# Kernel optimization log

Hardware: AMD Instinct MI355X
Metric: run time of the kernel (lower is better)

## Reference

```python
import jax, jax.numpy as jnp
import numpy as np


def setup_inputs() -> dict:
    key = jax.random.key(0)
    k1, k2 = jax.random.split(key)
    input_tensor = jax.random.normal(k1, (32, 128, 64, 64), dtype=jnp.float32)
    weights = jax.random.normal(k2, (256, 128, 3, 3), dtype=jnp.float32) * 0.05
    return {"input_tensor": input_tensor, "weights": weights}


def reference(input_tensor, weights):
    # Valid-padding, stride-1, no-bias direct conv2d (NCHW x OIHW -> NCHW),
    # identical math to the quintuple-loop slice*weight sum in the original.
    return jax.lax.conv_general_dilated(
        input_tensor,
        weights,
        window_strides=(1, 1),
        padding="VALID",
        dimension_numbers=("NCHW", "OIHW", "NCHW"),
    )
```

## Files before the change

kernel.cpp:

```cpp
#include <hip/hip_runtime.h>
#include <hip/hip_bf16.h>

#define N_IMG 32
#define CIN   128
#define INH   64
#define INW   64
#define COUT  256
#define OH    62
#define OW    62

typedef short          bf16x8 __attribute__((ext_vector_type(8)));
typedef unsigned short u16x8  __attribute__((ext_vector_type(8)));
typedef float          f32x4  __attribute__((ext_vector_type(4)));
typedef float          f32x2  __attribute__((ext_vector_type(2)));

__device__ __forceinline__ unsigned short f2bf(float x) {
    unsigned int u = __float_as_uint(x);
    u += 0x7fffu + ((u >> 16) & 1u);
    return (unsigned short)(u >> 16);
}

__device__ __forceinline__ void gload_lds16(const void* g, void* l) {
    __builtin_amdgcn_global_load_lds(
        (const __attribute__((address_space(1))) unsigned int*)g,
        (__attribute__((address_space(3))) unsigned int*)l, 16, 0, 0);
}

__global__ void wt_transform_kernel(const float* __restrict__ Wsrc,
                                    unsigned short* __restrict__ WT) {
    int idx = blockIdx.x * 256 + threadIdx.x;
    int i   = idx & 7;
    int co  = (idx >> 3) & 255;
    int cgk = idx >> 11;
    int cg  = cgk & 15;
    int khw = cgk >> 4;
    int kh  = khw / 3, kw = khw - 3 * kh;
    int ci  = cg * 8 + i;
    WT[idx] = f2bf(Wsrc[co * (CIN * 9) + ci * 9 + kh * 3 + kw]);
}

__global__ __launch_bounds__(256)
void in_transform_kernel(const float* __restrict__ In,
                         unsigned short* __restrict__ TIn) {
    __shared__ float T[32][66];
    const int bid = blockIdx.x;
    const int ih  = bid & 63;
    const int cb  = (bid >> 6) & 3;
    const int img = bid >> 8;

    {
        const int r  = threadIdx.x >> 3;
        const int c0 = (threadIdx.x & 7) * 8;
        const float* p = In + (((size_t)(img * CIN + cb * 32 + r)) * INH + ih) * INW + c0;
        f32x4 a = *(const f32x4*)p;
        f32x4 b = *(const f32x4*)(p + 4);
        *(f32x2*)&T[r][c0 + 0] = f32x2{a[0], a[1]};
        *(f32x2*)&T[r][c0 + 2] = f32x2{a[2], a[3]};
        *(f32x2*)&T[r][c0 + 4] = f32x2{b[0], b[1]};
        *(f32x2*)&T[r][c0 + 6] = f32x2{b[2], b[3]};
    }
    __syncthreads();

    const int c  = threadIdx.x;
    const int iw = c >> 2;
    const int cg = (c & 3) ^ ((iw >> 1) & 3);
    u16x8 v;
#pragma unroll
    for (int i = 0; i < 8; ++i) v[i] = f2bf(T[cg * 8 + i][iw]);
    *(u16x8*)&TIn[((size_t)bid * 256 + c) * 8] = v;
}

__global__ __launch_bounds__(256, 4)
void conv_mfma_bf16_kernel(const unsigned short* __restrict__ TIn,
                           const unsigned short* __restrict__ WT,
                           float* __restrict__ Out) {
    __shared__ unsigned short Lin[2][2112];

    const int g   = blockIdx.x;
    const int f   = (g & 7) * 248 + (g >> 3);
    const int img = f / OH;
    const int oh  = f - img * OH;

    const int tid  = threadIdx.x;
    const int wave = tid >> 6;
    const int lane = tid & 63;
    const int q    = lane >> 4;
    const int ml   = lane & 15;
    const int co_base = wave * 64;

    const unsigned short* tin_base = TIn + (size_t)img * (4 * 64 * 2048);
    const bf16x8* WTv = (const bf16x8*)WT;
    const int wlane = q * 256 + co_base + ml;

    int xoff[3][4];
#pragma unroll
    for (int kw = 0; kw < 3; ++kw)
#pragma unroll
        for (int ni = 0; ni < 4; ++ni) {
            const int r = ni * 16 + ml + kw;
            xoff[kw][ni] = r * 32 + ((q ^ ((r >> 1) & 3)) << 3);
        }

    f32x4 acc[4][4];
    const f32x4 zero = {0.f, 0.f, 0.f, 0.f};
#pragma unroll
    for (int a = 0; a < 4; ++a)
#pragma unroll
        for (int b = 0; b < 4; ++b) acc[a][b] = zero;

    gload_lds16(tin_base + oh * 2048 + tid * 8, &Lin[0][wave * 512]);
    if (tid < 64) ((unsigned int*)&Lin[tid >> 5][64 * 32])[tid & 31] = 0u;
    __syncthreads();

#pragma unroll
    for (int s = 0; s < 12; ++s) {
        const int cur = s & 1;
        if (s < 11) {
            const int s1 = s + 1;
            const unsigned short* src =
                tin_base + ((s1 & 3) * 64 + oh + (s1 >> 2)) * 2048;
            gload_lds16(src + tid * 8, &Lin[cur ^ 1][wave * 512]);
        }
        const int kh = s >> 2, cb = s & 3;
#pragma unroll
        for (int kw = 0; kw < 3; ++kw) {
            const int khw = kh * 3 + kw;
            const bf16x8* wbase = WTv + (khw * 16 + cb * 4) * 256;
            bf16x8 wf[4], xf[4];
#pragma unroll
            for (int mi = 0; mi < 4; ++mi)
                wf[mi] = wbase[wlane + mi * 16];
#pragma unroll
            for (int ni = 0; ni < 4; ++ni)
                xf[ni] = *(const bf16x8*)&Lin[cur][xoff[kw][ni]];
#pragma unroll
            for (int mi = 0; mi < 4; ++mi)
#pragma unroll
                for (int ni = 0; ni < 4; ++ni)
                    acc[mi][ni] = __builtin_amdgcn_mfma_f32_16x16x32_bf16(
                        wf[mi], xf[ni], acc[mi][ni], 0, 0, 0);
        }
        __syncthreads();
    }

#pragma unroll
    for (int mi = 0; mi < 4; ++mi) {
#pragma unroll
        for (int r = 0; r < 4; ++r) {
            const int co = co_base + mi * 16 + q * 4 + r;
            float* op = Out + ((img * COUT + co) * OH + oh) * OW;
#pragma unroll
            for (int ni = 0; ni < 4; ++ni) {
                const int ow = ni * 16 + ml;
                if (ow < OW) op[ow] = acc[mi][ni][r];
            }
        }
    }
}

__global__ __launch_bounds__(256, 2)
void conv_mfma_fp32_kernel(const float* __restrict__ In,
                           const unsigned short* __restrict__ WT,
                           float* __restrict__ Out) {
    __shared__ unsigned short Lin[66 * 32];

    const int oh   = blockIdx.x;
    const int img  = blockIdx.y;
    const int tid  = threadIdx.x;
    const int wave = tid >> 6;
    const int lane = tid & 63;
    const int q    = lane >> 4;
    const int ml   = lane & 15;
    const int co_base = wave * 64;

    f32x4 acc[4][4];
    const f32x4 zero = {0.f, 0.f, 0.f, 0.f};
#pragma unroll
    for (int a = 0; a < 4; ++a)
#pragma unroll
        for (int b = 0; b < 4; ++b) acc[a][b] = zero;

    if (tid < 32) ((unsigned int*)&Lin[64 * 32])[tid] = 0u;

    const int s_iw = tid & 63;
    const int s_cg = tid >> 6;
    const bf16x8* WTv = (const bf16x8*)WT;

    for (int kh = 0; kh < 3; ++kh) {
        const int ih = oh + kh;
        for (int cb = 0; cb < 4; ++cb) {
            const float* p = In + (((img * CIN + cb * 32 + s_cg * 8) * INH + ih) * INW + s_iw);
            u16x8 v;
#pragma unroll
            for (int i = 0; i < 8; ++i) v[i] = f2bf(p[i * (INH * INW)]);
            __syncthreads();
            *(u16x8*)&Lin[s_iw * 32 + ((s_cg ^ (s_iw & 3)) << 3)] = v;
            __syncthreads();

#pragma unroll
            for (int kw = 0; kw < 3; ++kw) {
                const int khw = kh * 3 + kw;
                bf16x8 wf[4], xf[4];
#pragma unroll
                for (int mi = 0; mi < 4; ++mi)
                    wf[mi] = WTv[(khw * 16 + cb * 4 + q) * 256 + co_base + mi * 16 + ml];
#pragma unroll
                for (int ni = 0; ni < 4; ++ni) {
                    const int row = ni * 16 + ml + kw;
                    xf[ni] = *(const bf16x8*)&Lin[row * 32 + ((q ^ (row & 3)) << 3)];
                }
#pragma unroll
                for (int mi = 0; mi < 4; ++mi)
#pragma unroll
                    for (int ni = 0; ni < 4; ++ni)
                        acc[mi][ni] = __builtin_amdgcn_mfma_f32_16x16x32_bf16(
                            wf[mi], xf[ni], acc[mi][ni], 0, 0, 0);
            }
        }
    }

#pragma unroll
    for (int mi = 0; mi < 4; ++mi) {
#pragma unroll
        for (int r = 0; r < 4; ++r) {
            const int co = co_base + mi * 16 + q * 4 + r;
            float* op = Out + ((img * COUT + co) * OH + oh) * OW;
#pragma unroll
            for (int ni = 0; ni < 4; ++ni) {
                const int ow = ni * 16 + ml;
                if (ow < OW) op[ow] = acc[mi][ni][r];
            }
        }
    }
}

__global__ void conv_naive_kernel(const float* __restrict__ In,
                                  const float* __restrict__ Wt,
                                  float* __restrict__ Out) {
    int idx = blockIdx.x * 256 + threadIdx.x;
    const int total = N_IMG * COUT * OH * OW;
    if (idx >= total) return;
    int ow = idx % OW; int t = idx / OW;
    int oh = t % OH;   t /= OH;
    int co = t % COUT; int img = t / COUT;
    float s = 0.f;
    for (int ci = 0; ci < CIN; ++ci)
#pragma unroll
        for (int kh = 0; kh < 3; ++kh)
#pragma unroll
            for (int kw = 0; kw < 3; ++kw)
                s += In[((img * CIN + ci) * INH + oh + kh) * INW + ow + kw] *
                     Wt[co * CIN * 9 + ci * 9 + kh * 3 + kw];
    Out[idx] = s;
}

extern "C" void kernel_launch(void* const* d_in, const int* in_sizes, int n_in,
                              void* d_out, int out_size, void* d_ws, size_t ws_size,
                              hipStream_t stream) {
    const float* In   = (const float*)d_in[0];
    const float* Wsrc = (const float*)d_in[1];
    float* Out        = (float*)d_out;

    const size_t WT_BYTES  = (size_t)9 * 16 * 256 * 8 * sizeof(unsigned short);
    const size_t TIN_BYTES = (size_t)N_IMG * 4 * 64 * 2048 * sizeof(unsigned short);

    if (ws_size >= WT_BYTES + TIN_BYTES) {
        unsigned short* WT  = (unsigned short*)d_ws;
        unsigned short* TIn = (unsigned short*)((char*)d_ws + WT_BYTES);
        wt_transform_kernel<<<dim3(294912 / 256), dim3(256), 0, stream>>>(Wsrc, WT);
        in_transform_kernel<<<dim3(N_IMG * 4 * 64), dim3(256), 0, stream>>>(In, TIn);
        conv_mfma_bf16_kernel<<<dim3(OH * N_IMG), dim3(256), 0, stream>>>(TIn, WT, Out);
    } else if (ws_size >= WT_BYTES) {
        unsigned short* WT = (unsigned short*)d_ws;
        wt_transform_kernel<<<dim3(294912 / 256), dim3(256), 0, stream>>>(Wsrc, WT);
        conv_mfma_fp32_kernel<<<dim3(OH, N_IMG), dim3(256), 0, stream>>>(In, WT, Out);
    } else {
        const int total = N_IMG * COUT * OH * OW;
        conv_naive_kernel<<<dim3((total + 255) / 256), dim3(256), 0, stream>>>(In, Wsrc, Out);
    }
}
```

Baseline: 242.0 us.

## Merge transform kernels and stage three input rows per LDS pipeline step

The weight and input transform kernels are merged into one launch, with block ranges split by blockIdx, which removes a kernel launch and the gap between them. The conv kernel now loads all three kh rows for a channel block into LDS at once, so the pipeline runs 4 stages instead of 12. That cuts barriers and gives more MFMA work per stage to hide load latency. The cost is triple the LDS per block, about 25 KB, which may lower occupancy below the 4 blocks per CU the launch bounds ask for.

Result: slower. 267.3 us (+10.5%).

```diff
diff --git a/kernel.cpp b/kernel.cpp
--- a/kernel.cpp
+++ b/kernel.cpp
@@ -9,6 +9,9 @@
 #define OH    62
 #define OW    62
 
+#define IN_BLOCKS (N_IMG * 4 * 64)
+#define WT_BLOCKS (294912 / 256)
+
 typedef short          bf16x8 __attribute__((ext_vector_type(8)));
 typedef unsigned short u16x8  __attribute__((ext_vector_type(8)));
 typedef float          f32x4  __attribute__((ext_vector_type(4)));
@@ -24,6 +27,145 @@
     __builtin_amdgcn_global_load_lds(
         (const __attribute__((address_space(1))) unsigned int*)g,
         (__attribute__((address_space(3))) unsigned int*)l, 16, 0, 0);
+}
+
+__global__ __launch_bounds__(256)
+void transform_kernel(const float* __restrict__ In,
+                      const float* __restrict__ Wsrc,
+                      unsigned short* __restrict__ TIn,
+                      unsigned short* __restrict__ WT) {
+    if (blockIdx.x >= IN_BLOCKS) {
+        int idx = (blockIdx.x - IN_BLOCKS) * 256 + threadIdx.x;
+        int i   = idx & 7;
+        int co  = (idx >> 3) & 255;
+        int cgk = idx >> 11;
+        int cg  = cgk & 15;
+        int khw = cgk >> 4;
+        int kh  = khw / 3, kw = khw - 3 * kh;
+        int ci  = cg * 8 + i;
+        WT[idx] = f2bf(Wsrc[co * (CIN * 9) + ci * 9 + kh * 3 + kw]);
+        return;
+    }
+    __shared__ float T[32][66];
+    const int bid = blockIdx.x;
+    const int ih  = bid & 63;
+    const int cb  = (bid >> 6) & 3;
+    const int img = bid >> 8;
+    {
+        const int r  = threadIdx.x >> 3;
+        const int c0 = (threadIdx.x & 7) * 8;
+        const float* p = In + (((size_t)(img * CIN + cb * 32 + r)) * INH + ih) * INW + c0;
+        f32x4 a = *(const f32x4*)p;
+        f32x4 b = *(const f32x4*)(p + 4);
+        *(f32x2*)&T[r][c0 + 0] = f32x2{a[0], a[1]};
+        *(f32x2*)&T[r][c0 + 2] = f32x2{a[2], a[3]};
+        *(f32x2*)&T[r][c0 + 4] = f32x2{b[0], b[1]};
+        *(f32x2*)&T[r][c0 + 6] = f32x2{b[2], b[3]};
+    }
+    __syncthreads();
+    const int c  = threadIdx.x;
+    const int iw = c >> 2;
+    const int cg = (c & 3) ^ ((iw >> 1) & 3);
+    u16x8 v;
+#pragma unroll
+    for (int i = 0; i < 8; ++i) v[i] = f2bf(T[cg * 8 + i][iw]);
+    *(u16x8*)&TIn[((size_t)bid * 256 + c) * 8] = v;
+}
+
+__global__ __launch_bounds__(256, 4)
+void conv_mfma_bf16_kernel(const unsigned short* __restrict__ TIn,
+                           const unsigned short* __restrict__ WT,
+                           float* __restrict__ Out) {
+    __shared__ unsigned short Lin[2][3][2112];
+
+    const int g   = blockIdx.x;
+    const int f   = (g & 7) * 248 + (g >> 3);
+    const int img = f / OH;
+    const int oh  = f - img * OH;
+
+    const int tid  = threadIdx.x;
+    const int wave = tid >> 6;
+    const int lane = tid & 63;
+    const int q    = lane >> 4;
+    const int ml   = lane & 15;
+    const int co_base = wave * 64;
+
+    const unsigned short* tin_base = TIn + (size_t)img * (4 * 64 * 2048);
+    const bf16x8* WTv = (const bf16x8*)WT;
+    const int wlane = q * 256 + co_base + ml;
+
+    int xoff[3][4];
+#pragma unroll
+    for (int kw = 0; kw < 3; ++kw)
+#pragma unroll
+        for (int ni = 0; ni < 4; ++ni) {
+            const int r = ni * 16 + ml + kw;
+            xoff[kw][ni] = r * 32 + ((q ^ ((r >> 1) & 3)) << 3);
+        }
+
+    f32x4 acc[4][4];
+    const f32x4 zero = {0.f, 0.f, 0.f, 0.f};
+#pragma unroll
+    for (int a = 0; a < 4; ++a)
+#pragma unroll
+        for (int b = 0; b < 4; ++b) acc[a][b] = zero;
+
+#pragma unroll
+    for (int j = 0; j < 3; ++j)
+        gload_lds16(tin_base + (oh + j) * 2048 + tid * 8, &Lin[0][j][wave * 512]);
+    if (tid < 192) {
+        const int rb = tid >> 5;
+        ((unsigned int*)Lin)[rb * 1056 + 1024 + (tid & 31)] = 0u;
+    }
+    __syncthreads();
+
+#pragma unroll
+    for (int cb = 0; cb < 4; ++cb) {
+        const int cur = cb & 1;
+        if (cb < 3) {
+            const unsigned short* src = tin_base + ((cb + 1) * 64 + oh) * 2048;
+#pragma unroll
+            for (int j = 0; j < 3; ++j)
+                gload_lds16(src + j * 2048 + tid * 8, &Lin[cur ^ 1][j][wave * 512]);
+        }
+#pragma unroll
+        for (int kh = 0; kh < 3; ++kh) {
+            const unsigned short* rowb = &Lin[cur][kh][0];
+#pragma unroll
+            for (int kw = 0; kw < 3; ++kw) {
+                const int khw = kh * 3 + kw;
+                const bf16x8* wbase = WTv + (khw * 16 + cb * 4) * 256;
+                bf16x8 wf[4], xf[4];
+#pragma unroll
+                for (int mi = 0; mi < 4; ++mi)
+                    wf[mi] = wbase[wlane + mi * 16];
+#pragma unroll
+                for (int ni = 0; ni < 4; ++ni)
+                    xf[ni] = *(const bf16x8*)&rowb[xoff[kw][ni]];
+#pragma unroll
+                for (int mi = 0; mi < 4; ++mi)
+#pragma unroll
+                    for (int ni = 0; ni < 4; ++ni)
+                        acc[mi][ni] = __builtin_amdgcn_mfma_f32_16x16x32_bf16(
+                            wf[mi], xf[ni], acc[mi][ni], 0, 0, 0);
+            }
+        }
+        __syncthreads();
+    }
+
+#pragma unroll
+    for (int mi = 0; mi < 4; ++mi) {
+#pragma unroll
+        for (int r = 0; r < 4; ++r) {
+            const int co = co_base + mi * 16 + q * 4 + r;
+            float* op = Out + ((img * COUT + co) * OH + oh) * OW;
+#pragma unroll
+            for (int ni = 0; ni < 4; ++ni) {
+                const int ow = ni * 16 + ml;
+                if (ow < OW) op[ow] = acc[mi][ni][r];
+            }
+        }
+    }
 }
 
 __global__ void wt_transform_kernel(const float* __restrict__ Wsrc,
@@ -39,125 +181,6 @@
     WT[idx] = f2bf(Wsrc[co * (CIN * 9) + ci * 9 + kh * 3 + kw]);
 }
 
-__global__ __launch_bounds__(256)
-void in_transform_kernel(const float* __restrict__ In,
-                         unsigned short* __restrict__ TIn) {
-    __shared__ float T[32][66];
-    const int bid = blockIdx.x;
-    const int ih  = bid & 63;
-    const int cb  = (bid >> 6) & 3;
-    const int img = bid >> 8;
-
-    {
-        const int r  = threadIdx.x >> 3;
-        const int c0 = (threadIdx.x & 7) * 8;
-        const float* p = In + (((size_t)(img * CIN + cb * 32 + r)) * INH + ih) * INW + c0;
-        f32x4 a = *(const f32x4*)p;
-        f32x4 b = *(const f32x4*)(p + 4);
-        *(f32x2*)&T[r][c0 + 0] = f32x2{a[0], a[1]};
-        *(f32x2*)&T[r][c0 + 2] = f32x2{a[2], a[3]};
-        *(f32x2*)&T[r][c0 + 4] = f32x2{b[0], b[1]};
-        *(f32x2*)&T[r][c0 + 6] = f32x2{b[2], b[3]};
-    }
-    __syncthreads();
-
-    const int c  = threadIdx.x;
-    const int iw = c >> 2;
-    const int cg = (c & 3) ^ ((iw >> 1) & 3);
-    u16x8 v;
-#pragma unroll
-    for (int i = 0; i < 8; ++i) v[i] = f2bf(T[cg * 8 + i][iw]);
-    *(u16x8*)&TIn[((size_t)bid * 256 + c) * 8] = v;
-}
-
-__global__ __launch_bounds__(256, 4)
-void conv_mfma_bf16_kernel(const unsigned short* __restrict__ TIn,
-                           const unsigned short* __restrict__ WT,
-                           float* __restrict__ Out) {
-    __shared__ unsigned short Lin[2][2112];
-
-    const int g   = blockIdx.x;
-    const int f   = (g & 7) * 248 + (g >> 3);
-    const int img = f / OH;
-    const int oh  = f - img * OH;
-
-    const int tid  = threadIdx.x;
-    const int wave = tid >> 6;
-    const int lane = tid & 63;
-    const int q    = lane >> 4;
-    const int ml   = lane & 15;
-    const int co_base = wave * 64;
-
-    const unsigned short* tin_base = TIn + (size_t)img * (4 * 64 * 2048);
-    const bf16x8* WTv = (const bf16x8*)WT;
-    const int wlane = q * 256 + co_base + ml;
-
-    int xoff[3][4];
-#pragma unroll
-    for (int kw = 0; kw < 3; ++kw)
-#pragma unroll
-        for (int ni = 0; ni < 4; ++ni) {
-            const int r = ni * 16 + ml + kw;
-            xoff[kw][ni] = r * 32 + ((q ^ ((r >> 1) & 3)) << 3);
-        }
-
-    f32x4 acc[4][4];
-    const f32x4 zero = {0.f, 0.f, 0.f, 0.f};
-#pragma unroll
-    for (int a = 0; a < 4; ++a)
-#pragma unroll
-        for (int b = 0; b < 4; ++b) acc[a][b] = zero;
-
-    gload_lds16(tin_base + oh * 2048 + tid * 8, &Lin[0][wave * 512]);
-    if (tid < 64) ((unsigned int*)&Lin[tid >> 5][64 * 32])[tid & 31] = 0u;
-    __syncthreads();
-
-#pragma unroll
-    for (int s = 0; s < 12; ++s) {
-        const int cur = s & 1;
-        if (s < 11) {
-            const int s1 = s + 1;
-            const unsigned short* src =
-                tin_base + ((s1 & 3) * 64 + oh + (s1 >> 2)) * 2048;
-            gload_lds16(src + tid * 8, &Lin[cur ^ 1][wave * 512]);
-        }
-        const int kh = s >> 2, cb = s & 3;
-#pragma unroll
-        for (int kw = 0; kw < 3; ++kw) {
-            const int khw = kh * 3 + kw;
-            const bf16x8* wbase = WTv + (khw * 16 + cb * 4) * 256;
-            bf16x8 wf[4], xf[4];
-#pragma unroll
-            for (int mi = 0; mi < 4; ++mi)
-                wf[mi] = wbase[wlane + mi * 16];
-#pragma unroll
-            for (int ni = 0; ni < 4; ++ni)
-                xf[ni] = *(const bf16x8*)&Lin[cur][xoff[kw][ni]];
-#pragma unroll
-            for (int mi = 0; mi < 4; ++mi)
-#pragma unroll
-                for (int ni = 0; ni < 4; ++ni)
-                    acc[mi][ni] = __builtin_amdgcn_mfma_f32_16x16x32_bf16(
-                        wf[mi], xf[ni], acc[mi][ni], 0, 0, 0);
-        }
-        __syncthreads();
-    }
-
-#pragma unroll
-    for (int mi = 0; mi < 4; ++mi) {
-#pragma unroll
-        for (int r = 0; r < 4; ++r) {
-            const int co = co_base + mi * 16 + q * 4 + r;
-            float* op = Out + ((img * COUT + co) * OH + oh) * OW;
-#pragma unroll
-            for (int ni = 0; ni < 4; ++ni) {
-                const int ow = ni * 16 + ml;
-                if (ow < OW) op[ow] = acc[mi][ni][r];
-            }
-        }
-    }
-}
-
 __global__ __launch_bounds__(256, 2)
 void conv_mfma_fp32_kernel(const float* __restrict__ In,
                            const unsigned short* __restrict__ WT,
@@ -267,12 +290,11 @@
     if (ws_size >= WT_BYTES + TIN_BYTES) {
         unsigned short* WT  = (unsigned short*)d_ws;
         unsigned short* TIn = (unsigned short*)((char*)d_ws + WT_BYTES);
-        wt_transform_kernel<<<dim3(294912 / 256), dim3(256), 0, stream>>>(Wsrc, WT);
-        in_transform_kernel<<<dim3(N_IMG * 4 * 64), dim3(256), 0, stream>>>(In, TIn);
+        transform_kernel<<<dim3(IN_BLOCKS + WT_BLOCKS), dim3(256), 0, stream>>>(In, Wsrc, TIn, WT);
         conv_mfma_bf16_kernel<<<dim3(OH * N_IMG), dim3(256), 0, stream>>>(TIn, WT, Out);
     } else if (ws_size >= WT_BYTES) {
         unsigned short* WT = (unsigned short*)d_ws;
-        wt_transform_kernel<<<dim3(294912 / 256), dim3(256), 0, stream>>>(Wsrc, WT);
+        wt_transform_kernel<<<dim3(WT_BLOCKS), dim3(256), 0, stream>>>(Wsrc, WT);
         conv_mfma_fp32_kernel<<<dim3(OH, N_IMG), dim3(256), 0, stream>>>(In, WT, Out);
     } else {
         const int total = N_IMG * COUT * OH * OW;
```
